# Optimization experiments

Measured on AMD Instinct MI355X. Metric: run time of the kernel, lower is better.

Reference implementation:

```python
import jax, jax.numpy as jnp
import numpy as np

T, D, H = 8192, 128, 1024  # seq_len, obs_dim, lstm_hidden_size


def setup_inputs() -> dict:
    key = jax.random.key(0)
    ks = jax.random.split(key, 9)
    lim = 1.0 / np.sqrt(H)  # eqx LSTMCell/Linear uniform init scale

    def u(k, shape):
        return jax.random.uniform(k, shape, minval=-lim, maxval=lim, dtype=jnp.float32)

    obs = jax.random.normal(ks[0], (T, D), dtype=jnp.float32)
    W_ih0 = u(ks[1], (4 * H, D))
    W_hh0 = u(ks[2], (4 * H, H))
    b0 = u(ks[3], (4 * H,))
    W_ih1 = u(ks[4], (4 * H, H))
    W_hh1 = u(ks[5], (4 * H, H))
    b1 = u(ks[6], (4 * H,))
    W_dec = u(ks[7], (2 * D, H))
    b_dec = u(ks[8], (2 * D,))
    return {"obs": obs, "W_ih0": W_ih0, "W_hh0": W_hh0, "b0": b0,
            "W_ih1": W_ih1, "W_hh1": W_hh1, "b1": b1,
            "W_dec": W_dec, "b_dec": b_dec}


def _lstm_cell(gx, h, c, W_hh):
    # gx: (4H,) precomputed input projection + bias; h, c: (H,)
    z = gx + W_hh @ h
    i, f, g, o = jnp.split(z, 4)
    i = jax.nn.sigmoid(i)
    f = jax.nn.sigmoid(f)
    g = jnp.tanh(g)
    o = jax.nn.sigmoid(o)
    c_new = f * c + i * g
    h_new = o * jnp.tanh(c_new)
    return h_new, c_new


def reference(obs, W_ih0, W_hh0, b0, W_ih1, W_hh1, b1, W_dec, b_dec):
    d = obs.shape[1]
    hdim = W_hh0.shape[1]
    # teacher forcing: input at step t is obs[t-1], obs[-1] replaced by zeros
    shifted = jnp.concatenate([jnp.zeros((1, d), obs.dtype), obs[:-1]], axis=0)
    # layer-0 input projection is input-only -> precompute as one big GEMM (T, 4H)
    gx0_all = shifted @ W_ih0.T + b0

    def step(state, gx0_t):
        (h0, c0), (h1, c1) = state
        h0, c0 = _lstm_cell(gx0_t, h0, c0, W_hh0)
        gx1 = W_ih1 @ h0 + b1
        h1, c1 = _lstm_cell(gx1, h1, c1, W_hh1)
        return ((h0, c0), (h1, c1)), h1

    z = jnp.zeros((hdim,), obs.dtype)
    init = ((z, z), (z, z))
    _, all_h = jax.lax.scan(step, init, gx0_all)  # all_h: (T, H)

    params = all_h @ W_dec.T + b_dec  # (T, 2D)
    loc = params[:, :d]
    scale = jax.nn.softplus(params[:, d:]) + 1e-4
    return loc, scale
```

## Files before the change

### kernel.cpp

```cpp
#include <hip/hip_runtime.h>
#include <math.h>

#define TT 8192
#define DD 128
#define HH 1024
#define RINGN 64
#define NA 64
#define NB 128
#define NC 16
#define NWG (NA + NB + NC)


typedef unsigned long long ull;

__device__ __forceinline__ ull ldpair(const ull* p) {
  return __hip_atomic_load(p, __ATOMIC_RELAXED, __HIP_MEMORY_SCOPE_AGENT);
}
__device__ __forceinline__ void stpair(ull* p, float v, unsigned e) {
  ull u = ((ull)e << 32) | (ull)__float_as_uint(v);
  __hip_atomic_store(p, u, __ATOMIC_RELAXED, __HIP_MEMORY_SCOPE_AGENT);
}
__device__ __forceinline__ unsigned ldflag(const unsigned* p) {
  return __hip_atomic_load(p, __ATOMIC_RELAXED, __HIP_MEMORY_SCOPE_AGENT);
}
__device__ __forceinline__ void stflag(unsigned* p, unsigned v) {
  __hip_atomic_store(p, v, __ATOMIC_RELAXED, __HIP_MEMORY_SCOPE_AGENT);
}
__device__ __forceinline__ float sigm(float x) { return 1.0f / (1.0f + expf(-x)); }
__device__ __forceinline__ float softplusf(float x) {
  return x > 0.0f ? x + log1pf(expf(-x)) : log1pf(expf(x));
}

#define FMA16(W)                                                      \
  a0 = fmaf(W[0][4*i+0], h4.x, a0); a0 = fmaf(W[0][4*i+1], h4.y, a0); \
  a0 = fmaf(W[0][4*i+2], h4.z, a0); a0 = fmaf(W[0][4*i+3], h4.w, a0); \
  a1 = fmaf(W[1][4*i+0], h4.x, a1); a1 = fmaf(W[1][4*i+1], h4.y, a1); \
  a1 = fmaf(W[1][4*i+2], h4.z, a1); a1 = fmaf(W[1][4*i+3], h4.w, a1); \
  a2 = fmaf(W[2][4*i+0], h4.x, a2); a2 = fmaf(W[2][4*i+1], h4.y, a2); \
  a2 = fmaf(W[2][4*i+2], h4.z, a2); a2 = fmaf(W[2][4*i+3], h4.w, a2); \
  a3 = fmaf(W[3][4*i+0], h4.x, a3); a3 = fmaf(W[3][4*i+1], h4.y, a3); \
  a3 = fmaf(W[3][4*i+2], h4.z, a3); a3 = fmaf(W[3][4*i+3], h4.w, a3);

__global__ void __launch_bounds__(512, 1) deepar_persistent(
    const float* __restrict__ obs,
    const float* __restrict__ Wih0, const float* __restrict__ Whh0, const float* __restrict__ b0,
    const float* __restrict__ Wih1, const float* __restrict__ Whh1, const float* __restrict__ b1,
    const float* __restrict__ Wdec, const float* __restrict__ bdec,
    float* __restrict__ out,
    unsigned* b_cons, unsigned* c_cons,
    ull* h0_ring, ull* h1_ring)
{
  __shared__ __align__(16) float hx[2][2304];

  const int wg  = blockIdx.x;
  const int tid = threadIdx.x;

  if (wg < NA) {
    const int rg = tid >> 5;
    const int q  = tid & 31;
    const int j  = wg * 16 + rg;
    const int k0 = q * 36;
    float w[4][36];
    #pragma unroll
    for (int i = 0; i < 9; ++i) {
      const int kb = k0 + 4 * i;
      #pragma unroll
      for (int r = 0; r < 4; ++r) {
        const float* src = (kb < HH) ? (Whh0 + (size_t)(r * HH + j) * HH + kb)
                                     : (Wih0 + (size_t)(r * HH + j) * DD + (kb - HH));
        const float4 v = *(const float4*)src;
        w[r][4*i+0] = v.x; w[r][4*i+1] = v.y; w[r][4*i+2] = v.z; w[r][4*i+3] = v.w;
      }
    }
    float bs[4];
    #pragma unroll
    for (int r = 0; r < 4; ++r) bs[r] = b0[r * HH + j];
    float creg = 0.0f;

    for (int t = 0; t < TT; ++t) {
      float a0 = 0.f, a1 = 0.f, a2 = 0.f, a3 = 0.f;
      if (t > 0) {
        const float* obr = obs + (size_t)(t - 1) * DD;
        #pragma unroll
        for (int i = 0; i < 9; ++i) {
          const int kb = k0 + 4 * i;
          if (kb >= HH) { const float4 h4 = *(const float4*)(obr + (kb - HH)); FMA16(w) }
        }
      }
      if (((t & 15) == 0) && t >= 48 && tid < 64) {
        const unsigned need = (unsigned)(t - 32);
        while (!__all((ldflag(&b_cons[tid]) >= need) &
                      (ldflag(&b_cons[tid + 64]) >= need))) {}
      }
      float* Lb = hx[t & 1];
      {
        const ull* sl = h0_ring + (size_t)((t - 1) & (RINGN - 1)) * HH;
        const unsigned ee = (unsigned)t;
        bool d0 = false, d1 = false;
        do {
          ull u0 = 0, u1 = 0;
          if (!d0) u0 = ldpair(sl + tid);
          if (!d1) u1 = ldpair(sl + tid + 512);
          if (!d0 && (unsigned)(u0 >> 32) == ee) { Lb[tid]       = __uint_as_float((unsigned)u0); d0 = true; }
          if (!d1 && (unsigned)(u1 >> 32) == ee) { Lb[tid + 512] = __uint_as_float((unsigned)u1); d1 = true; }
        } while (!(d0 & d1));
      }
      __syncthreads();
      #pragma unroll
      for (int i = 0; i < 9; ++i) {
        const int kb = k0 + 4 * i;
        if (kb < HH) { const float4 h4 = *(const float4*)&Lb[kb]; FMA16(w) }
      }
      #pragma unroll
      for (int s = 1; s < 32; s <<= 1) {
        a0 += __shfl_xor(a0, s); a1 += __shfl_xor(a1, s);
        a2 += __shfl_xor(a2, s); a3 += __shfl_xor(a3, s);
      }
      if (q == 0) {
        const float ig = sigm(a0 + bs[0]);
        const float fg = sigm(a1 + bs[1]);
        const float gg = tanhf(a2 + bs[2]);
        const float og = sigm(a3 + bs[3]);
        creg = fg * creg + ig * gg;
        stpair(&h0_ring[(size_t)(t & (RINGN - 1)) * HH + j], og * tanhf(creg),
               (unsigned)(t + 1));
      }
    }

  } else if (wg < NA + NB) {
    const int rg = tid >> 6;
    const int q  = tid & 63;
    const int s_ = wg - NA;
    const int j  = s_ * 8 + rg;
    const int k0 = q * 32;
    float w[4][32];
    #pragma unroll
    for (int i = 0; i < 8; ++i) {
      const int kb = k0 + 4 * i;
      #pragma unroll
      for (int r = 0; r < 4; ++r) {
        const float* src = (kb < HH) ? (Wih1 + (size_t)(r * HH + j) * HH + kb)
                                     : (Whh1 + (size_t)(r * HH + j) * HH + (kb - HH));
        const float4 v = *(const float4*)src;
        w[r][4*i+0] = v.x; w[r][4*i+1] = v.y; w[r][4*i+2] = v.z; w[r][4*i+3] = v.w;
      }
    }
    float bs[4];
    #pragma unroll
    for (int r = 0; r < 4; ++r) bs[r] = b1[r * HH + j];
    float creg = 0.0f;
    const int p0 = tid + 4 * (tid >> 5);
    const int p1 = p0 + 576;
    const int p2 = p0 + 1152;
    const int p3 = p2 + 576;

    for (int t = 0; t < TT; ++t) {
      if (((t & 15) == 0) && t >= 48 && tid < 64) {
        const unsigned need = (unsigned)(t - 32);
        while (!__all((tid >= NC) | (ldflag(&c_cons[tid]) >= need))) {}
      }
      float* Lb = hx[t & 1];
      {
        const ull* s0 = h0_ring + (size_t)(t & (RINGN - 1)) * HH;
        const ull* s1 = h1_ring + (size_t)((t - 1) & (RINGN - 1)) * HH;
        const unsigned e0 = (unsigned)(t + 1);
        const unsigned e1 = (unsigned)t;
        bool d0 = false, d1 = false, d2 = false, d3 = false;
        do {
          ull u0 = 0, u1 = 0, u2 = 0, u3 = 0;
          if (!d0) u0 = ldpair(s0 + tid);
          if (!d1) u1 = ldpair(s0 + tid + 512);
          if (!d2) u2 = ldpair(s1 + tid);
          if (!d3) u3 = ldpair(s1 + tid + 512);
          if (!d0 && (unsigned)(u0 >> 32) == e0) { Lb[p0] = __uint_as_float((unsigned)u0); d0 = true; }
          if (!d1 && (unsigned)(u1 >> 32) == e0) { Lb[p1] = __uint_as_float((unsigned)u1); d1 = true; }
          if (!d2 && (unsigned)(u2 >> 32) == e1) { Lb[p2] = __uint_as_float((unsigned)u2); d2 = true; }
          if (!d3 && (unsigned)(u3 >> 32) == e1) { Lb[p3] = __uint_as_float((unsigned)u3); d3 = true; }
        } while (!(d0 & d1 & d2 & d3));
      }
      __syncthreads();
      if (tid == 0) stflag(&b_cons[s_], (unsigned)(t + 1));
      float a0 = 0.f, a1 = 0.f, a2 = 0.f, a3 = 0.f;
      {
        const int base = q * 36;
        #pragma unroll
        for (int i = 0; i < 8; ++i) {
          const float4 h4 = *(const float4*)&Lb[base + 4 * i];
          FMA16(w)
        }
      }
      #pragma unroll
      for (int s = 1; s < 64; s <<= 1) {
        a0 += __shfl_xor(a0, s); a1 += __shfl_xor(a1, s);
        a2 += __shfl_xor(a2, s); a3 += __shfl_xor(a3, s);
      }
      if (q == 0) {
        const float ig = sigm(a0 + bs[0]);
        const float fg = sigm(a1 + bs[1]);
        const float gg = tanhf(a2 + bs[2]);
        const float og = sigm(a3 + bs[3]);
        creg = fg * creg + ig * gg;
        stpair(&h1_ring[(size_t)(t & (RINGN - 1)) * HH + j], og * tanhf(creg),
               (unsigned)(t + 1));
      }
    }

  } else {
    const int rg = tid >> 6;
    const int q  = tid & 63;
    const int cg = wg - NA - NB;
    const int rowbase = cg * 16;
    const int row0 = rowbase + 2 * rg;
    const int k0 = q * 16;
    float w[2][16];
    #pragma unroll
    for (int i = 0; i < 4; ++i) {
      const int kb = k0 + 4 * i;
      #pragma unroll
      for (int r = 0; r < 2; ++r) {
        const float4 v = *(const float4*)(Wdec + (size_t)(row0 + r) * HH + kb);
        w[r][4*i+0] = v.x; w[r][4*i+1] = v.y; w[r][4*i+2] = v.z; w[r][4*i+3] = v.w;
      }
    }
    const float bs0 = bdec[row0], bs1 = bdec[row0 + 1];
    const int pc0 = tid + 4 * (tid >> 4);
    const int pc1 = pc0 + 640;

    for (int t = 0; t < TT; ++t) {
      float* Lb = hx[t & 1];
      {
        const ull* sl = h1_ring + (size_t)(t & (RINGN - 1)) * HH;
        const unsigned ee = (unsigned)(t + 1);
        bool d0 = false, d1 = false;
        do {
          ull u0 = 0, u1 = 0;
          if (!d0) u0 = ldpair(sl + tid);
          if (!d1) u1 = ldpair(sl + tid + 512);
          if (!d0 && (unsigned)(u0 >> 32) == ee) { Lb[pc0] = __uint_as_float((unsigned)u0); d0 = true; }
          if (!d1 && (unsigned)(u1 >> 32) == ee) { Lb[pc1] = __uint_as_float((unsigned)u1); d1 = true; }
        } while (!(d0 & d1));
      }
      __syncthreads();
      if (tid == 0) stflag(&c_cons[cg], (unsigned)(t + 1));
      float a0 = 0.f, a1 = 0.f;
      {
        const int base = q * 20;
        #pragma unroll
        for (int i = 0; i < 4; ++i) {
          const float4 h4 = *(const float4*)&Lb[base + 4 * i];
          a0 = fmaf(w[0][4*i+0], h4.x, a0); a0 = fmaf(w[0][4*i+1], h4.y, a0);
          a0 = fmaf(w[0][4*i+2], h4.z, a0); a0 = fmaf(w[0][4*i+3], h4.w, a0);
          a1 = fmaf(w[1][4*i+0], h4.x, a1); a1 = fmaf(w[1][4*i+1], h4.y, a1);
          a1 = fmaf(w[1][4*i+2], h4.z, a1); a1 = fmaf(w[1][4*i+3], h4.w, a1);
        }
      }
      #pragma unroll
      for (int s = 1; s < 64; s <<= 1) { a0 += __shfl_xor(a0, s); a1 += __shfl_xor(a1, s); }
      if (q == 0) {
        const float z0 = a0 + bs0;
        const float z1 = a1 + bs1;
        if (row0 < DD) {
          out[(size_t)t * DD + row0]     = z0;
          out[(size_t)t * DD + row0 + 1] = z1;
        } else {
          out[(size_t)TT * DD + (size_t)t * DD + (row0 - DD)]     = softplusf(z0) + 1e-4f;
          out[(size_t)TT * DD + (size_t)t * DD + (row0 - DD) + 1] = softplusf(z1) + 1e-4f;
        }
      }
    }
  }
}

extern "C" void kernel_launch(void* const* d_in, const int* in_sizes, int n_in,
                              void* d_out, int out_size, void* d_ws, size_t ws_size,
                              hipStream_t stream) {
  const float* obs  = (const float*)d_in[0];
  const float* Wih0 = (const float*)d_in[1];
  const float* Whh0 = (const float*)d_in[2];
  const float* b0   = (const float*)d_in[3];
  const float* Wih1 = (const float*)d_in[4];
  const float* Whh1 = (const float*)d_in[5];
  const float* b1   = (const float*)d_in[6];
  const float* Wdec = (const float*)d_in[7];
  const float* bdec = (const float*)d_in[8];
  float* out = (float*)d_out;

  unsigned char* ws = (unsigned char*)d_ws;
  unsigned* b_cons = (unsigned*)(ws);
  unsigned* c_cons = (unsigned*)(ws + 512);
  ull* h0_ring = (ull*)(ws + 4096);
  ull* h1_ring = (ull*)(ws + 4096 + (size_t)RINGN * HH * 8);

  hipMemsetAsync(ws, 0, 4096 + (size_t)2 * RINGN * HH * 8, stream);

  hipLaunchKernelGGL(deepar_persistent, dim3(NWG), dim3(512), 0, stream,
                     obs, Wih0, Whh0, b0, Wih1, Whh1, b1, Wdec, bdec, out,
                     b_cons, c_cons, h0_ring, h1_ring);
}
```

Before: 32.21 ms.

## Add ring-watcher workgroups that publish per-step ready flags for consumers

Adds two dedicated workgroups that each poll a whole h0 or h1 ring slot until every element carries the current epoch, then publish a step-ready counter replicated across eight cache lines. Consumer workgroups spin with s_sleep on a single flag before reading the ring, instead of every thread repeatedly re-polling tagged pairs across the whole ring. The goal is less polling traffic on shared ring lines and less memory contention. The cost is an extra hop in the critical recurrent path, since consumers now wait for the watcher's flag, plus sleep granularity.

After: 28.45 ms. 11.7% less time.

```diff
diff --git a/kernel.cpp b/kernel.cpp
--- a/kernel.cpp
+++ b/kernel.cpp
@@ -8,7 +8,8 @@
 #define NA 64
 #define NB 128
 #define NC 16
-#define NWG (NA + NB + NC)
+#define NR 2
+#define NWG (NA + NB + NC + NR)
 
 
 typedef unsigned long long ull;
@@ -47,13 +48,14 @@
     const float* __restrict__ Wih1, const float* __restrict__ Whh1, const float* __restrict__ b1,
     const float* __restrict__ Wdec, const float* __restrict__ bdec,
     float* __restrict__ out,
-    unsigned* b_cons, unsigned* c_cons,
+    unsigned* b_cons, unsigned* c_cons, unsigned* ready0, unsigned* ready1,
     ull* h0_ring, ull* h1_ring)
 {
   __shared__ __align__(16) float hx[2][2304];
 
   const int wg  = blockIdx.x;
   const int tid = threadIdx.x;
+  const int rc  = (wg & 7) * 16;
 
   if (wg < NA) {
     const int rg = tid >> 5;
@@ -92,6 +94,7 @@
         while (!__all((ldflag(&b_cons[tid]) >= need) &
                       (ldflag(&b_cons[tid + 64]) >= need))) {}
       }
+      if (t > 0) while (ldflag(&ready0[rc]) < (unsigned)t) __builtin_amdgcn_s_sleep(1);
       float* Lb = hx[t & 1];
       {
         const ull* sl = h0_ring + (size_t)((t - 1) & (RINGN - 1)) * HH;
@@ -159,6 +162,9 @@
         const unsigned need = (unsigned)(t - 32);
         while (!__all((tid >= NC) | (ldflag(&c_cons[tid]) >= need))) {}
       }
+      while (ldflag(&ready0[rc]) < (unsigned)(t + 1)) __builtin_amdgcn_s_sleep(1);
+      if (t > 0)
+        while (ldflag(&ready1[rc]) < (unsigned)t) __builtin_amdgcn_s_sleep(1);
       float* Lb = hx[t & 1];
       {
         const ull* s0 = h0_ring + (size_t)(t & (RINGN - 1)) * HH;
@@ -205,12 +211,11 @@
       }
     }
 
-  } else {
+  } else if (wg < NA + NB + NC) {
     const int rg = tid >> 6;
     const int q  = tid & 63;
     const int cg = wg - NA - NB;
-    const int rowbase = cg * 16;
-    const int row0 = rowbase + 2 * rg;
+    const int row0 = cg * 16 + 2 * rg;
     const int k0 = q * 16;
     float w[2][16];
     #pragma unroll
@@ -227,6 +232,7 @@
     const int pc1 = pc0 + 640;
 
     for (int t = 0; t < TT; ++t) {
+      while (ldflag(&ready1[rc]) < (unsigned)(t + 1)) __builtin_amdgcn_s_sleep(1);
       float* Lb = hx[t & 1];
       {
         const ull* sl = h1_ring + (size_t)(t & (RINGN - 1)) * HH;
@@ -266,6 +272,27 @@
           out[(size_t)TT * DD + (size_t)t * DD + (row0 - DD)]     = softplusf(z0) + 1e-4f;
           out[(size_t)TT * DD + (size_t)t * DD + (row0 - DD) + 1] = softplusf(z1) + 1e-4f;
         }
+      }
+    }
+
+  } else {
+    ull* ring      = (wg == NA + NB + NC) ? h0_ring : h1_ring;
+    unsigned* rdy  = (wg == NA + NB + NC) ? ready0  : ready1;
+    for (int t = 0; t < TT; ++t) {
+      const ull* sl = ring + (size_t)(t & (RINGN - 1)) * HH;
+      const unsigned ee = (unsigned)(t + 1);
+      bool d0 = false, d1 = false;
+      do {
+        ull u0 = 0, u1 = 0;
+        if (!d0) u0 = ldpair(sl + tid);
+        if (!d1) u1 = ldpair(sl + tid + 512);
+        d0 = d0 || ((unsigned)(u0 >> 32) == ee);
+        d1 = d1 || ((unsigned)(u1 >> 32) == ee);
+      } while (!(d0 & d1));
+      __syncthreads();
+      if (tid < 8) {
+        asm volatile("" ::: "memory");
+        stflag(&rdy[tid * 16], ee);
       }
     }
   }
@@ -288,6 +315,8 @@
   unsigned char* ws = (unsigned char*)d_ws;
   unsigned* b_cons = (unsigned*)(ws);
   unsigned* c_cons = (unsigned*)(ws + 512);
+  unsigned* ready0 = (unsigned*)(ws + 1024);
+  unsigned* ready1 = (unsigned*)(ws + 2048);
   ull* h0_ring = (ull*)(ws + 4096);
   ull* h1_ring = (ull*)(ws + 4096 + (size_t)RINGN * HH * 8);
 
@@ -295,5 +324,5 @@
 
   hipLaunchKernelGGL(deepar_persistent, dim3(NWG), dim3(512), 0, stream,
                      obs, Wih0, Whh0, b0, Wih1, Whh1, b1, Wdec, bdec, out,
-                     b_cons, c_cons, h0_ring, h1_ring);
-}
+                     b_cons, c_cons, ready0, ready1, h0_ring, h1_ring);
+}
```

## Dedicate single-wave pollers per ring and duplicate hidden-state rings per consumer

Applied to the files above, without the earlier changes.

Each workgroup now polls hidden-state rings with a single wavefront that sweeps 16 contiguous slots per lane, instead of all 512 threads polling in parallel. The other waves sit at the barrier, and the flow-control flag checks move to separate waves so they can overlap with polling. Producers write each hidden value into two separate rings (h0A/h0B, h1B/h1C) so that different consumer groups poll different cache lines. The aim is to cut polling traffic and contention on the shared rings, at the cost of extra stores, twice the workspace, and a longer serial sweep per lane.

Result: slower. 56.70 ms (+76.0%).

```diff
diff --git a/kernel.cpp b/kernel.cpp
--- a/kernel.cpp
+++ b/kernel.cpp
@@ -29,6 +29,23 @@
 __device__ __forceinline__ float sigm(float x) { return 1.0f / (1.0f + expf(-x)); }
 __device__ __forceinline__ float softplusf(float x) {
   return x > 0.0f ? x + log1pf(expf(-x)) : log1pf(expf(x));
+}
+
+__device__ __forceinline__ void sweep16(const ull* sl, int base, unsigned ee,
+                                        float* lds, const int* pos) {
+  unsigned pend = 0xFFFFu;
+  do {
+    #pragma unroll
+    for (int i = 0; i < 16; ++i) {
+      if (pend & (1u << i)) {
+        const ull u = ldpair(sl + base + i);
+        if ((unsigned)(u >> 32) == ee) {
+          lds[pos[i]] = __uint_as_float((unsigned)u);
+          pend &= ~(1u << i);
+        }
+      }
+    }
+  } while (pend);
 }
 
 #define FMA16(W)                                                      \
@@ -48,12 +65,14 @@
     const float* __restrict__ Wdec, const float* __restrict__ bdec,
     float* __restrict__ out,
     unsigned* b_cons, unsigned* c_cons,
-    ull* h0_ring, ull* h1_ring)
+    ull* h0A, ull* h0B, ull* h1B, ull* h1C)
 {
   __shared__ __align__(16) float hx[2][2304];
 
-  const int wg  = blockIdx.x;
-  const int tid = threadIdx.x;
+  const int wg   = blockIdx.x;
+  const int tid  = threadIdx.x;
+  const int wid  = tid >> 6;
+  const int lane = tid & 63;
 
   if (wg < NA) {
     const int rg = tid >> 5;
@@ -76,6 +95,9 @@
     #pragma unroll
     for (int r = 0; r < 4; ++r) bs[r] = b0[r * HH + j];
     float creg = 0.0f;
+    int pos[16];
+    #pragma unroll
+    for (int i = 0; i < 16; ++i) pos[i] = lane * 16 + i;
 
     for (int t = 0; t < TT; ++t) {
       float a0 = 0.f, a1 = 0.f, a2 = 0.f, a3 = 0.f;
@@ -87,29 +109,22 @@
           if (kb >= HH) { const float4 h4 = *(const float4*)(obr + (kb - HH)); FMA16(w) }
         }
       }
-      if (((t & 15) == 0) && t >= 48 && tid < 64) {
+      if (wid == 1 && ((t & 15) == 0) && t >= 48) {
         const unsigned need = (unsigned)(t - 32);
-        while (!__all((ldflag(&b_cons[tid]) >= need) &
-                      (ldflag(&b_cons[tid + 64]) >= need))) {}
+        while (!__all((ldflag(&b_cons[lane]) >= need) &
+                      (ldflag(&b_cons[lane + 64]) >= need))) {}
       }
       float* Lb = hx[t & 1];
-      {
-        const ull* sl = h0_ring + (size_t)((t - 1) & (RINGN - 1)) * HH;
-        const unsigned ee = (unsigned)t;
-        bool d0 = false, d1 = false;
-        do {
-          ull u0 = 0, u1 = 0;
-          if (!d0) u0 = ldpair(sl + tid);
-          if (!d1) u1 = ldpair(sl + tid + 512);
-          if (!d0 && (unsigned)(u0 >> 32) == ee) { Lb[tid]       = __uint_as_float((unsigned)u0); d0 = true; }
-          if (!d1 && (unsigned)(u1 >> 32) == ee) { Lb[tid + 512] = __uint_as_float((unsigned)u1); d1 = true; }
-        } while (!(d0 & d1));
-      }
+      if (wid == 0 && t > 0)
+        sweep16(h0A + (size_t)((t - 1) & (RINGN - 1)) * HH, lane * 16,
+                (unsigned)t, Lb, pos);
       __syncthreads();
-      #pragma unroll
-      for (int i = 0; i < 9; ++i) {
-        const int kb = k0 + 4 * i;
-        if (kb < HH) { const float4 h4 = *(const float4*)&Lb[kb]; FMA16(w) }
+      if (t > 0) {
+        #pragma unroll
+        for (int i = 0; i < 9; ++i) {
+          const int kb = k0 + 4 * i;
+          if (kb < HH) { const float4 h4 = *(const float4*)&Lb[kb]; FMA16(w) }
+        }
       }
       #pragma unroll
       for (int s = 1; s < 32; s <<= 1) {
@@ -122,8 +137,11 @@
         const float gg = tanhf(a2 + bs[2]);
         const float og = sigm(a3 + bs[3]);
         creg = fg * creg + ig * gg;
-        stpair(&h0_ring[(size_t)(t & (RINGN - 1)) * HH + j], og * tanhf(creg),
-               (unsigned)(t + 1));
+        const float hv = og * tanhf(creg);
+        const size_t off = (size_t)(t & (RINGN - 1)) * HH + j;
+        const unsigned ep = (unsigned)(t + 1);
+        stpair(&h0A[off], hv, ep);
+        stpair(&h0B[off], hv, ep);
       }
     }
 
@@ -149,45 +167,40 @@
     #pragma unroll
     for (int r = 0; r < 4; ++r) bs[r] = b1[r * HH + j];
     float creg = 0.0f;
-    const int p0 = tid + 4 * (tid >> 5);
-    const int p1 = p0 + 576;
-    const int p2 = p0 + 1152;
-    const int p3 = p2 + 576;
+    int posH0[16], posH1[16];
+    #pragma unroll
+    for (int i = 0; i < 16; ++i) {
+      const int m = lane * 16 + i;
+      posH0[i] = m + 4 * (m >> 5);
+      posH1[i] = 1152 + m + 4 * (m >> 5);
+    }
+    const int baseB = (q < 32) ? q * 36 : 1152 + (q - 32) * 36;
 
     for (int t = 0; t < TT; ++t) {
-      if (((t & 15) == 0) && t >= 48 && tid < 64) {
+      if (wid == 2 && ((t & 15) == 0) && t >= 48) {
         const unsigned need = (unsigned)(t - 32);
-        while (!__all((tid >= NC) | (ldflag(&c_cons[tid]) >= need))) {}
+        while (!__all((lane >= NC) | (ldflag(&c_cons[lane]) >= need))) {}
       }
       float* Lb = hx[t & 1];
-      {
-        const ull* s0 = h0_ring + (size_t)(t & (RINGN - 1)) * HH;
-        const ull* s1 = h1_ring + (size_t)((t - 1) & (RINGN - 1)) * HH;
-        const unsigned e0 = (unsigned)(t + 1);
-        const unsigned e1 = (unsigned)t;
-        bool d0 = false, d1 = false, d2 = false, d3 = false;
-        do {
-          ull u0 = 0, u1 = 0, u2 = 0, u3 = 0;
-          if (!d0) u0 = ldpair(s0 + tid);
-          if (!d1) u1 = ldpair(s0 + tid + 512);
-          if (!d2) u2 = ldpair(s1 + tid);
-          if (!d3) u3 = ldpair(s1 + tid + 512);
-          if (!d0 && (unsigned)(u0 >> 32) == e0) { Lb[p0] = __uint_as_float((unsigned)u0); d0 = true; }
-          if (!d1 && (unsigned)(u1 >> 32) == e0) { Lb[p1] = __uint_as_float((unsigned)u1); d1 = true; }
-          if (!d2 && (unsigned)(u2 >> 32) == e1) { Lb[p2] = __uint_as_float((unsigned)u2); d2 = true; }
-          if (!d3 && (unsigned)(u3 >> 32) == e1) { Lb[p3] = __uint_as_float((unsigned)u3); d3 = true; }
-        } while (!(d0 & d1 & d2 & d3));
+      if (wid == 0) {
+        if (t > 0)
+          sweep16(h1B + (size_t)((t - 1) & (RINGN - 1)) * HH, lane * 16,
+                  (unsigned)t, Lb, posH1);
+        else {
+          #pragma unroll
+          for (int i = 0; i < 16; ++i) Lb[posH1[i]] = 0.0f;
+        }
+      } else if (wid == 1) {
+        sweep16(h0B + (size_t)(t & (RINGN - 1)) * HH, lane * 16,
+                (unsigned)(t + 1), Lb, posH0);
       }
       __syncthreads();
       if (tid == 0) stflag(&b_cons[s_], (unsigned)(t + 1));
       float a0 = 0.f, a1 = 0.f, a2 = 0.f, a3 = 0.f;
-      {
-        const int base = q * 36;
-        #pragma unroll
-        for (int i = 0; i < 8; ++i) {
-          const float4 h4 = *(const float4*)&Lb[base + 4 * i];
-          FMA16(w)
-        }
+      #pragma unroll
+      for (int i = 0; i < 8; ++i) {
+        const float4 h4 = *(const float4*)&Lb[baseB + 4 * i];
+        FMA16(w)
       }
       #pragma unroll
       for (int s = 1; s < 64; s <<= 1) {
@@ -200,8 +213,11 @@
         const float gg = tanhf(a2 + bs[2]);
         const float og = sigm(a3 + bs[3]);
         creg = fg * creg + ig * gg;
-        stpair(&h1_ring[(size_t)(t & (RINGN - 1)) * HH + j], og * tanhf(creg),
-               (unsigned)(t + 1));
+        const float hv = og * tanhf(creg);
+        const size_t off = (size_t)(t & (RINGN - 1)) * HH + j;
+        const unsigned ep = (unsigned)(t + 1);
+        stpair(&h1B[off], hv, ep);
+        stpair(&h1C[off], hv, ep);
       }
     }
 
@@ -209,8 +225,7 @@
     const int rg = tid >> 6;
     const int q  = tid & 63;
     const int cg = wg - NA - NB;
-    const int rowbase = cg * 16;
-    const int row0 = rowbase + 2 * rg;
+    const int row0 = cg * 16 + 2 * rg;
     const int k0 = q * 16;
     float w[2][16];
     #pragma unroll
@@ -223,23 +238,15 @@
       }
     }
     const float bs0 = bdec[row0], bs1 = bdec[row0 + 1];
-    const int pc0 = tid + 4 * (tid >> 4);
-    const int pc1 = pc0 + 640;
+    int pos[16];
+    #pragma unroll
+    for (int i = 0; i < 16; ++i) pos[i] = lane * 20 + i;
 
     for (int t = 0; t < TT; ++t) {
       float* Lb = hx[t & 1];
-      {
-        const ull* sl = h1_ring + (size_t)(t & (RINGN - 1)) * HH;
-        const unsigned ee = (unsigned)(t + 1);
-        bool d0 = false, d1 = false;
-        do {
-          ull u0 = 0, u1 = 0;
-          if (!d0) u0 = ldpair(sl + tid);
-          if (!d1) u1 = ldpair(sl + tid + 512);
-          if (!d0 && (unsigned)(u0 >> 32) == ee) { Lb[pc0] = __uint_as_float((unsigned)u0); d0 = true; }
-          if (!d1 && (unsigned)(u1 >> 32) == ee) { Lb[pc1] = __uint_as_float((unsigned)u1); d1 = true; }
-        } while (!(d0 & d1));
-      }
+      if (wid == 0)
+        sweep16(h1C + (size_t)(t & (RINGN - 1)) * HH, lane * 16,
+                (unsigned)(t + 1), Lb, pos);
       __syncthreads();
       if (tid == 0) stflag(&c_cons[cg], (unsigned)(t + 1));
       float a0 = 0.f, a1 = 0.f;
@@ -285,15 +292,18 @@
   const float* bdec = (const float*)d_in[8];
   float* out = (float*)d_out;
 
+  const size_t RB = (size_t)RINGN * HH * 8;
   unsigned char* ws = (unsigned char*)d_ws;
   unsigned* b_cons = (unsigned*)(ws);
   unsigned* c_cons = (unsigned*)(ws + 512);
-  ull* h0_ring = (ull*)(ws + 4096);
-  ull* h1_ring = (ull*)(ws + 4096 + (size_t)RINGN * HH * 8);
-
-  hipMemsetAsync(ws, 0, 4096 + (size_t)2 * RINGN * HH * 8, stream);
+  ull* h0A = (ull*)(ws + 4096);
+  ull* h0B = (ull*)(ws + 4096 + RB);
+  ull* h1B = (ull*)(ws + 4096 + 2 * RB);
+  ull* h1C = (ull*)(ws + 4096 + 3 * RB);
+
+  hipMemsetAsync(ws, 0, 4096 + 4 * RB, stream);
 
   hipLaunchKernelGGL(deepar_persistent, dim3(NWG), dim3(512), 0, stream,
                      obs, Wih0, Whh0, b0, Wih1, Whh1, b1, Wdec, bdec, out,
-                     b_cons, c_cons, h0_ring, h1_ring);
-}
+                     b_cons, c_cons, h0A, h0B, h1B, h1C);
+}
```
